# Kernel optimization log

Hardware: AMD Instinct MI355X
Metric: run time of the kernel (lower is better)

The kernel has to match this reference:

```python
import jax, jax.numpy as jnp
import numpy as np

HEADS = 16
DIM_HEAD = 64
QUERY_DIM = 1024
CONTEXT_DIM = 1024
INNER = HEADS * DIM_HEAD  # 1024


def setup_inputs() -> dict:
    key = jax.random.key(0)
    k1, k2, k3, k4, k5, k6, k7 = jax.random.split(key, 7)
    B, N, M = 4, 2048, 2048
    s = 0.02
    return {
        "x": jax.random.normal(k1, (B, N, QUERY_DIM), jnp.float32),
        "context": jax.random.normal(k2, (B, M, CONTEXT_DIM), jnp.float32),
        "Wq": jax.random.normal(k3, (INNER, QUERY_DIM), jnp.float32) * s,
        "Wk": jax.random.normal(k4, (INNER, CONTEXT_DIM), jnp.float32) * s,
        "Wv": jax.random.normal(k5, (INNER, CONTEXT_DIM), jnp.float32) * s,
        "Wo": jax.random.normal(k6, (QUERY_DIM, INNER), jnp.float32) * s,
        "bo": jax.random.normal(k7, (QUERY_DIM,), jnp.float32) * s,
    }


def reference(x, context, Wq, Wk, Wv, Wo, bo):
    B, N, _ = x.shape
    M = context.shape[1]
    scale = DIM_HEAD ** (-0.5)
    # projections (torch Linear: y = x @ W.T)
    q = jnp.einsum('bnd,ed->bne', x, Wq)
    k = jnp.einsum('bmd,ed->bme', context, Wk)
    v = jnp.einsum('bmd,ed->bme', context, Wv)
    # split heads: b n (h d) -> b h n d
    q = q.reshape(B, N, HEADS, DIM_HEAD).transpose(0, 2, 1, 3)
    k = k.reshape(B, M, HEADS, DIM_HEAD).transpose(0, 2, 1, 3)
    v = v.reshape(B, M, HEADS, DIM_HEAD).transpose(0, 2, 1, 3)
    sim = jnp.einsum('bhid,bhjd->bhij', q, k) * scale
    attn = jax.nn.softmax(sim, axis=-1)
    out = jnp.einsum('bhij,bhjd->bhid', attn, v)
    out = out.transpose(0, 2, 1, 3).reshape(B, N, INNER)
    return jnp.einsum('bne,oe->bno', out, Wo) + bo
```

## Files before the change

kernel.cpp:

```cpp
#include <hip/hip_runtime.h>
#include <hip/hip_bf16.h>
#include <stdint.h>

#define HEADS 16
#define DIMH  64
#define SEQN  2048
#define SEQM  2048
#define NB    4
#define EDIM  1024
#define KD    1024

using bf16_t = __bf16;
using bf16x8 = __attribute__((ext_vector_type(8))) bf16_t;
using f32x4  = __attribute__((ext_vector_type(4))) float;

__device__ __forceinline__ unsigned short f2bf(float f) {
  union { float f; uint32_t u; } v; v.f = f;
  uint32_t u = v.u;
  u += 0x7fffu + ((u >> 16) & 1u);
  return (unsigned short)(u >> 16);
}

#if __has_builtin(__builtin_amdgcn_cvt_pk_bf16_f32)
typedef __bf16 bf16x2_t __attribute__((ext_vector_type(2)));
__device__ __forceinline__ uint32_t pk_bf16(float a, float b) {
  union { bf16x2_t v; uint32_t u; } c;
  c.v = __builtin_amdgcn_cvt_pk_bf16_f32(a, b);
  return c.u;
}
#else
__device__ __forceinline__ uint32_t pk_bf16(float a, float b) {
  union { __hip_bfloat162 v; uint32_t u; } c;
  c.v = __float22bfloat162_rn(float2{a, b});
  return c.u;
}
#endif

#if __has_builtin(__builtin_amdgcn_exp2f)
__device__ __forceinline__ float fexp2(float x) { return __builtin_amdgcn_exp2f(x); }
#else
__device__ __forceinline__ float fexp2(float x) { return exp2f(x); }
#endif

__device__ __forceinline__ void async16(const void* g, void* l) {
  __builtin_amdgcn_global_load_lds(
      (__attribute__((address_space(1))) void*)(g),
      (__attribute__((address_space(3))) void*)(l), 16, 0, 0);
}

__device__ __forceinline__ bf16x8 ldsv(const unsigned short* p) {
  return *(const bf16x8*)p;
}

__global__ __launch_bounds__(256)
void cvt2(const float4* __restrict__ a, const float4* __restrict__ b,
          ushort4* __restrict__ oa, ushort4* __restrict__ ob, int blocks_per_seg) {
  const int seg = blockIdx.x / blocks_per_seg;
  const int i = (blockIdx.x - seg * blocks_per_seg) * 256 + threadIdx.x;
  const float4* in = seg ? b : a;
  ushort4* out = seg ? ob : oa;
  float4 v = in[i];
  ushort4 o;
  o.x = f2bf(v.x); o.y = f2bf(v.y); o.z = f2bf(v.z); o.w = f2bf(v.w);
  out[i] = o;
}

__global__ __launch_bounds__(256)
void cvt4(const float4* __restrict__ a, const float4* __restrict__ b,
          const float4* __restrict__ c, const float4* __restrict__ d,
          ushort4* __restrict__ oa, ushort4* __restrict__ ob,
          ushort4* __restrict__ oc, ushort4* __restrict__ od, int blocks_per_seg) {
  const int seg = blockIdx.x / blocks_per_seg;
  const int i = (blockIdx.x - seg * blocks_per_seg) * 256 + threadIdx.x;
  const float4* in = (seg == 0) ? a : (seg == 1) ? b : (seg == 2) ? c : d;
  ushort4* out = (seg == 0) ? oa : (seg == 1) ? ob : (seg == 2) ? oc : od;
  float4 v = in[i];
  ushort4 o;
  o.x = f2bf(v.x); o.y = f2bf(v.y); o.z = f2bf(v.z); o.w = f2bf(v.w);
  out[i] = o;
}

__global__ __launch_bounds__(256)
void gemm_qkv(const unsigned short* __restrict__ xb,
              const unsigned short* __restrict__ cb,
              const unsigned short* __restrict__ wqb,
              const unsigned short* __restrict__ wkb,
              const unsigned short* __restrict__ wvb,
              unsigned short* __restrict__ Qb,
              unsigned short* __restrict__ Kb,
              unsigned short* __restrict__ Vtb,
              float qscale)
{
  __shared__ __align__(16) unsigned short As[128 * 32];
  __shared__ __align__(16) unsigned short Bs[128 * 32];
  const int t   = threadIdx.x;
  const int wv  = t >> 6;
  const int ln  = t & 63;
  const int l15 = ln & 15;
  const int qd  = ln >> 4;
  const int z   = blockIdx.z;
  const int n0  = blockIdx.x * 128;
  const int m0  = blockIdx.y * 128;
  const int wm  = (wv >> 1) * 64;
  const int wn  = (wv & 1) * 64;

  const unsigned short* A = (z == 0) ? xb : cb;
  const unsigned short* W = (z == 0) ? wqb : (z == 1) ? wkb : wvb;

  const f32x4 vzero = {0.f, 0.f, 0.f, 0.f};
  f32x4 acc[4][4];
#pragma unroll
  for (int i = 0; i < 4; ++i)
#pragma unroll
    for (int j = 0; j < 4; ++j) acc[i][j] = vzero;

  for (int k0 = 0; k0 < KD; k0 += 32) {
    __syncthreads();
#pragma unroll
    for (int l = 0; l < 2; ++l) {
      const int i = l * 256 + wv * 64 + ln;
      const int row = i >> 2, ch = i & 3;
      async16(A + (size_t)(m0 + row) * KD + k0 + ch * 8, As + i * 8);
      async16(W + (size_t)(n0 + row) * KD + k0 + ch * 8, Bs + i * 8);
    }
    __syncthreads();
    bf16x8 af[4], bfr[4];
#pragma unroll
    for (int mt = 0; mt < 4; ++mt)
      af[mt] = ldsv(As + (wm + mt * 16 + l15) * 32 + qd * 8);
#pragma unroll
    for (int nt = 0; nt < 4; ++nt)
      bfr[nt] = ldsv(Bs + (wn + nt * 16 + l15) * 32 + qd * 8);
#pragma unroll
    for (int mt = 0; mt < 4; ++mt)
#pragma unroll
      for (int nt = 0; nt < 4; ++nt)
        acc[mt][nt] = __builtin_amdgcn_mfma_f32_16x16x32_bf16(af[mt], bfr[nt], acc[mt][nt], 0, 0, 0);
  }

  const float scale = (z == 0) ? qscale : 1.0f;
#pragma unroll
  for (int mt = 0; mt < 4; ++mt) {
#pragma unroll
    for (int nt = 0; nt < 4; ++nt) {
      const int col   = n0 + wn + nt * 16 + l15;
      const int rbase = m0 + wm + mt * 16 + qd * 4;
      if (z < 2) {
        unsigned short* outb = (z == 0) ? Qb : Kb;
#pragma unroll
        for (int r = 0; r < 4; ++r)
          outb[(size_t)(rbase + r) * EDIM + col] = f2bf(acc[mt][nt][r] * scale);
      } else {
        const int b = rbase >> 11, m = rbase & 2047;
        const int h = col >> 6,   d = col & 63;
        ushort4 o;
        o.x = f2bf(acc[mt][nt][0]); o.y = f2bf(acc[mt][nt][1]);
        o.z = f2bf(acc[mt][nt][2]); o.w = f2bf(acc[mt][nt][3]);
        *(ushort4*)(Vtb + ((size_t)(b * HEADS + h) * DIMH + d) * SEQM + m) = o;
      }
    }
  }
}

__global__ __launch_bounds__(256)
void gemm_out(const unsigned short* __restrict__ A,
              const unsigned short* __restrict__ W,
              float* __restrict__ outf,
              const float* __restrict__ bias)
{
  __shared__ __align__(16) unsigned short As[128 * 32];
  __shared__ __align__(16) unsigned short Bs[128 * 32];
  const int t   = threadIdx.x;
  const int wv  = t >> 6;
  const int ln  = t & 63;
  const int l15 = ln & 15;
  const int qd  = ln >> 4;
  const int n0  = blockIdx.x * 128;
  const int m0  = blockIdx.y * 128;
  const int wm  = (wv >> 1) * 64;
  const int wn  = (wv & 1) * 64;

  const f32x4 vzero = {0.f, 0.f, 0.f, 0.f};
  f32x4 acc[4][4];
#pragma unroll
  for (int i = 0; i < 4; ++i)
#pragma unroll
    for (int j = 0; j < 4; ++j) acc[i][j] = vzero;

  for (int k0 = 0; k0 < KD; k0 += 32) {
    __syncthreads();
#pragma unroll
    for (int l = 0; l < 2; ++l) {
      const int i = l * 256 + wv * 64 + ln;
      const int row = i >> 2, ch = i & 3;
      async16(A + (size_t)(m0 + row) * KD + k0 + ch * 8, As + i * 8);
      async16(W + (size_t)(n0 + row) * KD + k0 + ch * 8, Bs + i * 8);
    }
    __syncthreads();
    bf16x8 af[4], bfr[4];
#pragma unroll
    for (int mt = 0; mt < 4; ++mt)
      af[mt] = ldsv(As + (wm + mt * 16 + l15) * 32 + qd * 8);
#pragma unroll
    for (int nt = 0; nt < 4; ++nt)
      bfr[nt] = ldsv(Bs + (wn + nt * 16 + l15) * 32 + qd * 8);
#pragma unroll
    for (int mt = 0; mt < 4; ++mt)
#pragma unroll
      for (int nt = 0; nt < 4; ++nt)
        acc[mt][nt] = __builtin_amdgcn_mfma_f32_16x16x32_bf16(af[mt], bfr[nt], acc[mt][nt], 0, 0, 0);
  }

#pragma unroll
  for (int mt = 0; mt < 4; ++mt) {
#pragma unroll
    for (int nt = 0; nt < 4; ++nt) {
      const int col   = n0 + wn + nt * 16 + l15;
      const int rbase = m0 + wm + mt * 16 + qd * 4;
      const float bv = bias[col];
#pragma unroll
      for (int r = 0; r < 4; ++r)
        outf[(size_t)(rbase + r) * EDIM + col] = acc[mt][nt][r] + bv;
    }
  }
}

__global__ __launch_bounds__(256)
void attn_kernel(const unsigned short* __restrict__ Q,
                 const unsigned short* __restrict__ K,
                 const unsigned short* __restrict__ VT,
                 unsigned short* __restrict__ O)
{
  __shared__ __align__(16) unsigned short Qs[128 * 64];
  __shared__ __align__(16) unsigned short Ks[64 * 64];
  __shared__ __align__(16) unsigned short Vs[64 * 64];
  unsigned short* Ps = Qs;

  const int t   = threadIdx.x;
  const int wv  = t >> 6;
  const int ln  = t & 63;
  const int l15 = ln & 15;
  const int qd  = ln >> 4;

  const int L      = blockIdx.x;
  const int bh     = ((L >> 7) << 3) | (L & 7);
  const int qt     = (L >> 3) & 15;
  const int q0     = qt * 128;
  const int b      = bh >> 4;
  const int h      = bh & 15;

  const unsigned short* Qp = Q + (size_t)b * SEQN * EDIM + h * DIMH;
  const unsigned short* Kp = K + (size_t)b * SEQM * EDIM + h * DIMH;
  const unsigned short* Vp = VT + ((size_t)bh) * DIMH * SEQM;

#pragma unroll
  for (int l = 0; l < 4; ++l) {
    const int i = l * 256 + wv * 64 + ln;
    const int row = i >> 3, ch = i & 7;
    const int gch = ch ^ (row & 7);
    async16(Qp + (size_t)(q0 + row) * EDIM + gch * 8, Qs + i * 8);
  }
  __syncthreads();

  bf16x8 qf[2][2];
#pragma unroll
  for (int qc = 0; qc < 2; ++qc) {
    const int row = wv * 32 + qc * 16 + l15;
#pragma unroll
    for (int ks = 0; ks < 2; ++ks) {
      const int c = (ks * 4 + qd) ^ (row & 7);
      qf[qc][ks] = ldsv(Qs + row * 64 + c * 8);
    }
  }

  const unsigned short* kg[2];
  const unsigned short* vg[2];
  unsigned short* kls[2];
  unsigned short* vls[2];
#pragma unroll
  for (int l = 0; l < 2; ++l) {
    const int i = l * 256 + wv * 64 + ln;
    const int row = i >> 3, ch = i & 7;
    const int gch = ch ^ (row & 7);
    kg[l] = Kp + (size_t)row * EDIM + gch * 8;
    vg[l] = Vp + (size_t)row * SEQM + gch * 8;
    kls[l] = Ks + i * 8;
    vls[l] = Vs + i * 8;
  }

  const f32x4 vzero = {0.f, 0.f, 0.f, 0.f};
  f32x4 o_acc[2][4];
#pragma unroll
  for (int qc = 0; qc < 2; ++qc)
#pragma unroll
    for (int dt = 0; dt < 4; ++dt) o_acc[qc][dt] = vzero;

  float2 rs2[2] = {{0.f, 0.f}, {0.f, 0.f}};

  unsigned short* Pw = Ps + wv * 2048;

  for (int j0 = 0; j0 < SEQM; j0 += 64) {
    __syncthreads();
    async16(kg[0], kls[0]);
    async16(kg[1], kls[1]);
    async16(vg[0], vls[0]);
    async16(vg[1], vls[1]);
    kg[0] += 64 * EDIM; kg[1] += 64 * EDIM;
    vg[0] += 64;        vg[1] += 64;
    __syncthreads();

    f32x4 st[2][4];
#pragma unroll
    for (int qc = 0; qc < 2; ++qc)
#pragma unroll
      for (int jt = 0; jt < 4; ++jt) st[qc][jt] = vzero;

#pragma unroll
    for (int jt = 0; jt < 4; ++jt) {
      const int rowj = jt * 16 + l15;
#pragma unroll
      for (int ks = 0; ks < 2; ++ks) {
        const int c = (ks * 4 + qd) ^ (rowj & 7);
        const bf16x8 kf = ldsv(Ks + rowj * 64 + c * 8);
        st[0][jt] = __builtin_amdgcn_mfma_f32_16x16x32_bf16(kf, qf[0][ks], st[0][jt], 0, 0, 0);
        st[1][jt] = __builtin_amdgcn_mfma_f32_16x16x32_bf16(kf, qf[1][ks], st[1][jt], 0, 0, 0);
      }
    }

#pragma unroll
    for (int qc = 0; qc < 2; ++qc) {
      unsigned short* prow = Pw + (qc * 16 + l15) * 64;
#pragma unroll
      for (int jt = 0; jt < 4; ++jt) {
        float p0 = fexp2(st[qc][jt][0]);
        float p1 = fexp2(st[qc][jt][1]);
        float p2 = fexp2(st[qc][jt][2]);
        float p3 = fexp2(st[qc][jt][3]);
        rs2[qc].x += p0 + p2;
        rs2[qc].y += p1 + p3;
        uint2 dw;
        dw.x = pk_bf16(p0, p1);
        dw.y = pk_bf16(p2, p3);
        const int c = (jt * 4 + qd) ^ l15;
        *(uint2*)(prow + c * 4) = dw;
      }
    }
    asm volatile("" ::: "memory");

#pragma unroll
    for (int ks2 = 0; ks2 < 2; ++ks2) {
      bf16x8 pf[2];
#pragma unroll
      for (int qc = 0; qc < 2; ++qc) {
        const unsigned short* prow = Pw + (qc * 16 + l15) * 64;
        const int c0 = ks2 * 8 + qd * 2;
        uint2 lo = *(const uint2*)(prow + ((c0)     ^ l15) * 4);
        uint2 hi = *(const uint2*)(prow + ((c0 + 1) ^ l15) * 4);
        union { uint32_t u[4]; bf16x8 v; } cc;
        cc.u[0] = lo.x; cc.u[1] = lo.y; cc.u[2] = hi.x; cc.u[3] = hi.y;
        pf[qc] = cc.v;
      }
#pragma unroll
      for (int dt = 0; dt < 4; ++dt) {
        const int rowd = dt * 16 + l15;
        const int c = (ks2 * 4 + qd) ^ (rowd & 7);
        const bf16x8 vf = ldsv(Vs + rowd * 64 + c * 8);
        o_acc[0][dt] = __builtin_amdgcn_mfma_f32_16x16x32_bf16(pf[0], vf, o_acc[0][dt], 0, 0, 0);
        o_acc[1][dt] = __builtin_amdgcn_mfma_f32_16x16x32_bf16(pf[1], vf, o_acc[1][dt], 0, 0, 0);
      }
    }
  }

  float rsum[2];
#pragma unroll
  for (int qc = 0; qc < 2; ++qc) {
    float r = rs2[qc].x + rs2[qc].y;
    r += __shfl_xor(r, 16);
    r += __shfl_xor(r, 32);
    rsum[qc] = r;
  }

  unsigned short* Op = O + (size_t)b * SEQN * EDIM + h * DIMH;
#pragma unroll
  for (int qc = 0; qc < 2; ++qc) {
    float inv[4];
#pragma unroll
    for (int r = 0; r < 4; ++r)
      inv[r] = 1.0f / __shfl(rsum[qc], qd * 4 + r);
#pragma unroll
    for (int dt = 0; dt < 4; ++dt) {
      const int col = dt * 16 + l15;
#pragma unroll
      for (int r = 0; r < 4; ++r) {
        const int row = q0 + wv * 32 + qc * 16 + qd * 4 + r;
        Op[(size_t)row * EDIM + col] = f2bf(o_acc[qc][dt][r] * inv[r]);
      }
    }
  }
}

extern "C" void kernel_launch(void* const* d_in, const int* in_sizes, int n_in,
                              void* d_out, int out_size, void* d_ws, size_t ws_size,
                              hipStream_t stream) {
  const float* x   = (const float*)d_in[0];
  const float* ctx = (const float*)d_in[1];
  const float* Wq  = (const float*)d_in[2];
  const float* Wk  = (const float*)d_in[3];
  const float* Wv  = (const float*)d_in[4];
  const float* Wo  = (const float*)d_in[5];
  const float* bo  = (const float*)d_in[6];
  float* out = (float*)d_out;

  char* ws = (char*)d_ws;
  const size_t SZ_X = (size_t)NB * SEQN * EDIM * 2;
  const size_t SZ_W = (size_t)EDIM * KD * 2;
  unsigned short* xb  = (unsigned short*)(ws);
  unsigned short* cb  = (unsigned short*)(ws + SZ_X);
  unsigned short* wqb = (unsigned short*)(ws + 2 * SZ_X);
  unsigned short* wkb = (unsigned short*)(ws + 2 * SZ_X + SZ_W);
  unsigned short* wvb = (unsigned short*)(ws + 2 * SZ_X + 2 * SZ_W);
  unsigned short* wob = (unsigned short*)(ws + 2 * SZ_X + 3 * SZ_W);
  unsigned short* Qb  = (unsigned short*)(ws + 2 * SZ_X + 4 * SZ_W);
  unsigned short* Kb  = (unsigned short*)(ws + 3 * SZ_X + 4 * SZ_W);
  unsigned short* Vtb = (unsigned short*)(ws + 4 * SZ_X + 4 * SZ_W);
  unsigned short* Ob  = (unsigned short*)(ws + 5 * SZ_X + 4 * SZ_W);

  const int n4x = (NB * SEQN * EDIM) / 4;
  const int n4w = (EDIM * KD) / 4;
  const int bpx = n4x / 256;
  const int bpw = n4w / 256;
  cvt2<<<2 * bpx, 256, 0, stream>>>((const float4*)x, (const float4*)ctx,
                                    (ushort4*)xb, (ushort4*)cb, bpx);
  cvt4<<<4 * bpw, 256, 0, stream>>>((const float4*)Wq, (const float4*)Wk,
                                    (const float4*)Wv, (const float4*)Wo,
                                    (ushort4*)wqb, (ushort4*)wkb,
                                    (ushort4*)wvb, (ushort4*)wob, bpw);

  const float SCL2E = 0.125f * 1.4426950408889634f;
  const dim3 blk(256);

  gemm_qkv<<<dim3(EDIM / 128, (NB * SEQN) / 128, 3), blk, 0, stream>>>(
      xb, cb, wqb, wkb, wvb, Qb, Kb, Vtb, SCL2E);

  attn_kernel<<<dim3(1024), blk, 0, stream>>>(Qb, Kb, Vtb, Ob);

  gemm_out<<<dim3(EDIM / 128, (NB * SEQN) / 128), blk, 0, stream>>>(Ob, wob, out, bo);
}
```

Measured before the change: 345.4 us.

## Remap GEMM block indices for XCD-aware L2 locality and simplify attention loads

Both projection GEMMs now use a flattened 1D grid and a block-index remap so that consecutive blocks on the same XCD (round-robin by L&7) share the same A row tile while sweeping all N column tiles. This is meant to raise L2 reuse of the activation tiles within each XCD's private L2 on MI355X. The attention kernel drops precomputed K/V pointer registers in favour of recomputing addresses from j0 each iteration, and collapses the paired row-sum accumulators into a single scalar, which may lower register pressure but lengthens the dependency chain on the sum.

```diff
diff --git a/kernel.cpp b/kernel.cpp
--- a/kernel.cpp
+++ b/kernel.cpp
@@ -98,9 +98,14 @@
   const int ln  = t & 63;
   const int l15 = ln & 15;
   const int qd  = ln >> 4;
-  const int z   = blockIdx.z;
-  const int n0  = blockIdx.x * 128;
-  const int m0  = blockIdx.y * 128;
+
+  const int L   = blockIdx.x;
+  const int xcd = L & 7;
+  const int n0  = ((L >> 3) & 7) * 128;
+  const int mq  = (L >> 6) & 7;
+  const int z   = L >> 9;
+  const int m0  = (mq * 8 + xcd) * 128;
+
   const int wm  = (wv >> 1) * 64;
   const int wn  = (wv & 1) * 64;
 
@@ -175,8 +180,13 @@
   const int ln  = t & 63;
   const int l15 = ln & 15;
   const int qd  = ln >> 4;
-  const int n0  = blockIdx.x * 128;
-  const int m0  = blockIdx.y * 128;
+
+  const int L   = blockIdx.x;
+  const int xcd = L & 7;
+  const int n0  = ((L >> 3) & 7) * 128;
+  const int mq  = L >> 6;
+  const int m0  = (mq * 8 + xcd) * 128;
+
   const int wm  = (wv >> 1) * 64;
   const int wn  = (wv & 1) * 64;
 
@@ -273,21 +283,6 @@
     }
   }
 
-  const unsigned short* kg[2];
-  const unsigned short* vg[2];
-  unsigned short* kls[2];
-  unsigned short* vls[2];
-#pragma unroll
-  for (int l = 0; l < 2; ++l) {
-    const int i = l * 256 + wv * 64 + ln;
-    const int row = i >> 3, ch = i & 7;
-    const int gch = ch ^ (row & 7);
-    kg[l] = Kp + (size_t)row * EDIM + gch * 8;
-    vg[l] = Vp + (size_t)row * SEQM + gch * 8;
-    kls[l] = Ks + i * 8;
-    vls[l] = Vs + i * 8;
-  }
-
   const f32x4 vzero = {0.f, 0.f, 0.f, 0.f};
   f32x4 o_acc[2][4];
 #pragma unroll
@@ -295,18 +290,20 @@
 #pragma unroll
     for (int dt = 0; dt < 4; ++dt) o_acc[qc][dt] = vzero;
 
-  float2 rs2[2] = {{0.f, 0.f}, {0.f, 0.f}};
+  float rsum[2] = {0.f, 0.f};
 
   unsigned short* Pw = Ps + wv * 2048;
 
   for (int j0 = 0; j0 < SEQM; j0 += 64) {
     __syncthreads();
-    async16(kg[0], kls[0]);
-    async16(kg[1], kls[1]);
-    async16(vg[0], vls[0]);
-    async16(vg[1], vls[1]);
-    kg[0] += 64 * EDIM; kg[1] += 64 * EDIM;
-    vg[0] += 64;        vg[1] += 64;
+#pragma unroll
+    for (int l = 0; l < 2; ++l) {
+      const int i = l * 256 + wv * 64 + ln;
+      const int row = i >> 3, ch = i & 7;
+      const int gch = ch ^ (row & 7);
+      async16(Kp + (size_t)(j0 + row) * EDIM + gch * 8, Ks + i * 8);
+      async16(Vp + (size_t)row * SEQM + j0 + gch * 8, Vs + i * 8);
+    }
     __syncthreads();
 
     f32x4 st[2][4];
@@ -336,8 +333,7 @@
         float p1 = fexp2(st[qc][jt][1]);
         float p2 = fexp2(st[qc][jt][2]);
         float p3 = fexp2(st[qc][jt][3]);
-        rs2[qc].x += p0 + p2;
-        rs2[qc].y += p1 + p3;
+        rsum[qc] += (p0 + p1) + (p2 + p3);
         uint2 dw;
         dw.x = pk_bf16(p0, p1);
         dw.y = pk_bf16(p2, p3);
@@ -371,10 +367,9 @@
     }
   }
 
-  float rsum[2];
 #pragma unroll
   for (int qc = 0; qc < 2; ++qc) {
-    float r = rs2[qc].x + rs2[qc].y;
+    float r = rsum[qc];
     r += __shfl_xor(r, 16);
     r += __shfl_xor(r, 32);
     rsum[qc] = r;
@@ -439,10 +434,10 @@
   const float SCL2E = 0.125f * 1.4426950408889634f;
   const dim3 blk(256);
 
-  gemm_qkv<<<dim3(EDIM / 128, (NB * SEQN) / 128, 3), blk, 0, stream>>>(
+  gemm_qkv<<<dim3(1536), blk, 0, stream>>>(
       xb, cb, wqb, wkb, wvb, Qb, Kb, Vtb, SCL2E);
 
   attn_kernel<<<dim3(1024), blk, 0, stream>>>(Qb, Kb, Vtb, Ob);
 
-  gemm_out<<<dim3(EDIM / 128, (NB * SEQN) / 128), blk, 0, stream>>>(Ob, wob, out, bo);
-}
+  gemm_out<<<dim3(512), blk, 0, stream>>>(Ob, wob, out, bo);
+}
```

Measured after the change: 329.0 us. 1.05x faster.
